# Performance work log

Measured on AMD Instinct MI355X. Metric: run time of the kernel, lower is better.

Reference implementation:

```python
import jax, jax.numpy as jnp
import numpy as np

DT = 0.01  # init kwarg dt
M = 501    # microstructure feature length (hardcoded split [501, 501] in source)
H = 128    # hidden width


def _mlp(x, W1, b1, W2, b2):
    # Linear -> Softplus -> Linear
    return jax.nn.softplus(x @ W1 + b1) @ W2 + b2


def _linear_init(key, fan_in, fan_out):
    k1, k2 = jax.random.split(key)
    s = 1.0 / np.sqrt(fan_in)
    W = jax.random.uniform(k1, (fan_in, fan_out), minval=-s, maxval=s, dtype=jnp.float32)
    b = jax.random.uniform(k2, (fan_out,), minval=-s, maxval=s, dtype=jnp.float32)
    return W, b


def setup_inputs() -> dict:
    key = jax.random.key(0)
    ks = jax.random.split(key, 10)
    B, T = 32768, 512
    Ew1, Eb1 = _linear_init(ks[0], 2 * M, H)   # energy net: Linear(1002,128)
    Ew2, Eb2 = _linear_init(ks[1], H, 1)
    nw1, nb1 = _linear_init(ks[2], M, H)       # nu net: Linear(501,128)
    nw2, nb2 = _linear_init(ks[3], H, 1)
    bw1, bb1 = _linear_init(ks[4], 2 * M, H)   # beta net: Linear(1002,128)
    bw2, bb2 = _linear_init(ks[5], H, 1)
    e = jax.random.normal(ks[6], (B, T, 1), dtype=jnp.float32) * 0.01
    e_dot = jax.random.normal(ks[7], (B, T, 1), dtype=jnp.float32) * 0.01
    E = jax.random.uniform(ks[8], (B, M), dtype=jnp.float32)
    nu = jax.random.uniform(ks[9], (B, M), dtype=jnp.float32)
    return dict(e=e, e_dot=e_dot, E=E, nu=nu,
                Ew1=Ew1, Eb1=Eb1, Ew2=Ew2, Eb2=Eb2,
                nw1=nw1, nb1=nb1, nw2=nw2, nb2=nb2,
                bw1=bw1, bb1=bb1, bw2=bw2, bb2=bb2)


def reference(e, e_dot, E, nu,
              Ew1, Eb1, Ew2, Eb2,
              nw1, nb1, nw2, nb2,
              bw1, bb1, bw2, bb2):
    # microstructure encoder: m = concat(E, nu) -> [B, 1002]; constant over time,
    # so the three small MLPs are evaluated ONCE (the per-step autograd.grad of the
    # quadratic energy/dissipation potentials has closed form).
    m = jnp.concatenate((E, nu), axis=-1)
    Emod = jnp.exp(_mlp(m, Ew1, Eb1, Ew2, Eb2))                              # exp(E(m))    [B,1]
    nu_feat = m[:, M:]                                                        # second half of split
    nuv = jnp.exp(jnp.square(_mlp(nu_feat, nw1, nb1, nw2, nb2)) / 40000.0)    # exp(nu(.))   [B,1]
    beta = jnp.square(_mlp(m, bw1, bb1, bw2, bb2)) / 40000.0                  # beta(m)      [B,1]

    # Per-step closed-form derivatives of
    #   energy    = 1/2 exp(E(m)) u^2 + 1/2 (u - v)^2        (u = e_t, v = xi_t)
    #   potential = -1/2 exp(nu) p^2 + 1/2 sum(beta q^2)     (p = e_dot_t, q = -dE/dv = e_t - xi_t)
    #   s_eq = exp(E) u + (u - v);  s_neq = dPhi/dp = -exp(nu) p;  kinetics = dPhi/dq = beta q
    def step(xi, inputs):
        et, edt = inputs                     # [B,1] each
        q = et - xi
        stress_t = Emod * et + q + nuv * edt  # s_eq - s_neq
        xi_next = xi + DT * beta * q
        return xi_next, (stress_t, xi)

    xi0 = jnp.zeros_like(e[:, 0])            # [B,1]
    eT = jnp.moveaxis(e, 1, 0)               # [T,B,1]
    edT = jnp.moveaxis(e_dot, 1, 0)
    _, (stress, xi) = jax.lax.scan(step, xi0, (eT, edT))
    return jnp.moveaxis(stress, 0, 1), jnp.moveaxis(xi, 0, 1)  # [B,T,1] each
```

## Files before the change

### kernel.cpp

```cpp
#include <hip/hip_runtime.h>
#include <hip/hip_bf16.h>

#define M_ 501
#define NTOT 384
#define T_ 512
#define DT_ 0.01f

typedef __attribute__((ext_vector_type(8))) __bf16 bf16x8;
typedef __attribute__((ext_vector_type(4))) float f32x4;

static __device__ __forceinline__ unsigned int pack2(float a, float b) {
    __hip_bfloat16 ha = __float2bfloat16(a);
    __hip_bfloat16 hb = __float2bfloat16(b);
    unsigned short ua = __builtin_bit_cast(unsigned short, ha);
    unsigned short ub = __builtin_bit_cast(unsigned short, hb);
    return (unsigned int)ua | ((unsigned int)ub << 16);
}

__global__ void build_w(const float* __restrict__ Ew1, const float* __restrict__ bw1,
                        const float* __restrict__ nw1, __hip_bfloat16* __restrict__ Wswz) {
    int idx = blockIdx.x * 256 + threadIdx.x;
    if (idx >= 32 * 24 * 64 * 8) return;
    int e  = idx & 7;
    int l  = (idx >> 3) & 63;
    int t  = idx >> 9;
    int nt = t % 24, k0 = t / 24;
    int k  = k0 * 32 + ((l >> 4) << 3) + e;
    int n  = nt * 16 + (l & 15);
    float v = 0.f;
    if (n < 128)      { if (k < 2*M_)             v = Ew1[k * 128 + n]; }
    else if (n < 256) { if (k < 2*M_)             v = bw1[k * 128 + (n - 128)]; }
    else              { if (k >= M_ && k < 2*M_)  v = nw1[(k - M_) * 128 + (n - 256)]; }
    Wswz[idx] = __float2bfloat16(v);
}

__global__ __launch_bounds__(512, 4) void mlp_gemm_fused2(
    const float* __restrict__ E, const float* __restrict__ nu,
    const __hip_bfloat16* __restrict__ Wswz,
    const float* __restrict__ Eb1, const float* __restrict__ bb1, const float* __restrict__ nb1,
    const float* __restrict__ Ew2, const float* __restrict__ bw2, const float* __restrict__ nw2,
    const float* __restrict__ Eb2, const float* __restrict__ bb2, const float* __restrict__ nb2,
    float* __restrict__ Emod, float* __restrict__ nuv, float* __restrict__ beta, int B)
{
    const int tid = threadIdx.x;
    const int wid = tid >> 6, l = tid & 63;
    const int c = l & 15, g = l >> 4;
    const int brow = blockIdx.x * 32;

    __shared__ __align__(16) unsigned char sAraw[32 * 1024 * 2];

    #pragma unroll
    for (int it = 0; it < 8; ++it) {
        const int idx = tid + it * 512;
        const int r = idx >> 7, cu = idx & 127;
        const size_t rb = (size_t)(brow + r) * M_;
        float f0, f1, f2, f3, f4, f5, f6, f7;
        const bool slow = (cu == 62) | (cu >= 124);
        if (!slow) {
            const float* src = (cu < 62) ? E : nu;
            const int off = (cu < 62) ? cu * 8 : cu * 8 - M_;
            const size_t s = rb + (size_t)off;
            const int o = (int)(s & 3);
            const f32x4* p = (const f32x4*)(src + (s & ~(size_t)3));
            f32x4 q0 = p[0], q1 = p[1], q2 = p[2];
            asm volatile("" : "+v"(q0), "+v"(q1), "+v"(q2));
            float g0=q0[0], g1=q0[1], g2=q0[2], g3=q0[3],
                  g4=q1[0], g5=q1[1], g6=q1[2], g7=q1[3],
                  g8=q2[0], g9=q2[1], g10=q2[2];
            const bool o2 = (o & 2) != 0, o1 = (o & 1) != 0;
            float u0 = o2?g2:g0, u1 = o2?g3:g1, u2 = o2?g4:g2, u3 = o2?g5:g3,
                  u4 = o2?g6:g4, u5 = o2?g7:g5, u6 = o2?g8:g6, u7 = o2?g9:g7,
                  u8 = o2?g10:g8;
            f0 = o1?u1:u0; f1 = o1?u2:u1; f2 = o1?u3:u2; f3 = o1?u4:u3;
            f4 = o1?u5:u4; f5 = o1?u6:u5; f6 = o1?u7:u6; f7 = o1?u8:u7;
        } else {
            const int kb = cu * 8;
            auto ldx = [&](int k) -> float {
                return (k < M_) ? E[rb + k] : ((k < 2 * M_) ? nu[rb + k - M_] : 0.f);
            };
            f0 = ldx(kb+0); f1 = ldx(kb+1); f2 = ldx(kb+2); f3 = ldx(kb+3);
            f4 = ldx(kb+4); f5 = ldx(kb+5); f6 = ldx(kb+6); f7 = ldx(kb+7);
        }
        uint4 vv;
        vv.x = pack2(f0, f1); vv.y = pack2(f2, f3);
        vv.z = pack2(f4, f5); vv.w = pack2(f6, f7);
        const unsigned bo = ((unsigned)r << 11) + (((unsigned)cu << 4) ^ (((unsigned)(r & 7)) << 4));
        *(uint4*)(sAraw + bo) = vv;
    }
    __syncthreads();

    const bf16x8* wbase = (const bf16x8*)Wswz;
    f32x4 acc[2][3];
    #pragma unroll
    for (int mi = 0; mi < 2; mi++)
        #pragma unroll
        for (int nt = 0; nt < 3; nt++) acc[mi][nt] = (f32x4){0.f, 0.f, 0.f, 0.f};

    for (int k0 = 0; k0 < 32; ++k0) {
        bf16x8 af[2];
        #pragma unroll
        for (int mi = 0; mi < 2; mi++) {
            const int row = c + mi * 16;
            const unsigned bo = ((unsigned)row << 11) +
                ((((unsigned)k0 << 6) + ((unsigned)g << 4)) ^ (((unsigned)(row & 7)) << 4));
            af[mi] = *(const bf16x8*)(sAraw + bo);
        }
        #pragma unroll
        for (int nt = 0; nt < 3; nt++) {
            bf16x8 bfrag = wbase[(size_t)(k0 * 24 + wid * 3 + nt) * 64 + l];
            #pragma unroll
            for (int mi = 0; mi < 2; mi++)
                acc[mi][nt] = __builtin_amdgcn_mfma_f32_16x16x32_bf16(af[mi], bfrag, acc[mi][nt], 0, 0, 0);
        }
    }
    __syncthreads();

    float* lds_s = (float*)sAraw;
    if (tid < 96) lds_s[tid] = 0.f;
    __syncthreads();

    #pragma unroll
    for (int nt = 0; nt < 3; nt++) {
        int gnt = wid * 3 + nt;
        int mlp = gnt >> 3;
        int jj = (gnt * 16 + c) & 127;
        float b1 = (mlp == 0) ? Eb1[jj] : (mlp == 1) ? bb1[jj] : nb1[jj];
        float w2 = (mlp == 0) ? Ew2[jj] : (mlp == 1) ? bw2[jj] : nw2[jj];
        #pragma unroll
        for (int mi = 0; mi < 2; mi++) {
            #pragma unroll
            for (int r = 0; r < 4; r++) {
                float x = acc[mi][nt][r] + b1;
                float h = fmaxf(x, 0.f) + __logf(1.f + __expf(-fabsf(x)));
                float v = h * w2;
                v += __shfl_xor(v, 1);
                v += __shfl_xor(v, 2);
                v += __shfl_xor(v, 4);
                v += __shfl_xor(v, 8);
                if (c == 0) atomicAdd(&lds_s[mlp * 32 + mi * 16 + g * 4 + r], v);
            }
        }
    }
    __syncthreads();

    if (tid < 32) {
        int b = brow + tid;
        float s0 = lds_s[tid], s1 = lds_s[32 + tid], s2 = lds_s[64 + tid];
        Emod[b] = __expf(s0 + Eb2[0]);
        float mb = s1 + bb2[0];
        beta[b]  = mb * mb * (1.f / 40000.f);
        float mn = s2 + nb2[0];
        nuv[b]   = __expf(mn * mn * (1.f / 40000.f));
    }
}

__global__ __launch_bounds__(256) void scan_k(
    const float* __restrict__ e, const float* __restrict__ ed,
    const float* __restrict__ Emod, const float* __restrict__ nuv, const float* __restrict__ beta,
    float* __restrict__ stress, float* __restrict__ xiout)
{
    int lane = threadIdx.x & 63;
    int b = blockIdx.x * 4 + (threadIdx.x >> 6);
    float Em = Emod[b], nv = nuv[b], bt = beta[b];
    float cc = DT_ * bt;
    float a  = 1.f - cc;

    size_t base = (size_t)b * T_ + (size_t)lane * 8;
    float4 e0 = *(const float4*)(e + base),  e1 = *(const float4*)(e + base + 4);
    float4 d0 = *(const float4*)(ed + base), d1 = *(const float4*)(ed + base + 4);
    float ev[8] = {e0.x, e0.y, e0.z, e0.w, e1.x, e1.y, e1.z, e1.w};
    float dv[8] = {d0.x, d0.y, d0.z, d0.w, d1.x, d1.y, d1.z, d1.w};

    float S = 0.f;
    #pragma unroll
    for (int j = 0; j < 8; j++) S = a * S + ev[j];
    float a2 = a * a, a4 = a2 * a2, A = a4 * a4;

    #pragma unroll
    for (int d = 1; d < 64; d <<= 1) {
        float Su = __shfl_up(S, d);
        float Au = __shfl_up(A, d);
        if (lane >= d) { S = Su * A + S; A = Au * A; }
    }
    float Sp = __shfl_up(S, 1);
    float xi = (lane == 0) ? 0.f : cc * Sp;

    float st[8], xo[8];
    #pragma unroll
    for (int j = 0; j < 8; j++) {
        xo[j] = xi;
        float q = ev[j] - xi;
        st[j] = Em * ev[j] + q + nv * dv[j];
        xi = xi + cc * q;
    }
    *(float4*)(stress + base)     = (float4){st[0], st[1], st[2], st[3]};
    *(float4*)(stress + base + 4) = (float4){st[4], st[5], st[6], st[7]};
    *(float4*)(xiout + base)      = (float4){xo[0], xo[1], xo[2], xo[3]};
    *(float4*)(xiout + base + 4)  = (float4){xo[4], xo[5], xo[6], xo[7]};
}

extern "C" void kernel_launch(void* const* d_in, const int* in_sizes, int n_in,
                              void* d_out, int out_size, void* d_ws, size_t ws_size,
                              hipStream_t stream) {
    const float* e   = (const float*)d_in[0];
    const float* ed  = (const float*)d_in[1];
    const float* E   = (const float*)d_in[2];
    const float* nu  = (const float*)d_in[3];
    const float* Ew1 = (const float*)d_in[4];
    const float* Eb1 = (const float*)d_in[5];
    const float* Ew2 = (const float*)d_in[6];
    const float* Eb2 = (const float*)d_in[7];
    const float* nw1 = (const float*)d_in[8];
    const float* nb1 = (const float*)d_in[9];
    const float* nw2 = (const float*)d_in[10];
    const float* nb2 = (const float*)d_in[11];
    const float* bw1 = (const float*)d_in[12];
    const float* bb1 = (const float*)d_in[13];
    const float* bw2 = (const float*)d_in[14];
    const float* bb2 = (const float*)d_in[15];

    int B = in_sizes[2] / M_;

    char* ws = (char*)d_ws;
    __hip_bfloat16* Wswz = (__hip_bfloat16*)ws;
    float* Emod = (float*)(ws + (size_t)1024 * NTOT * 2);
    float* nuv  = Emod + B;
    float* beta = nuv + B;

    build_w<<<(1024 * NTOT + 255) / 256, 256, 0, stream>>>(Ew1, bw1, nw1, Wswz);
    mlp_gemm_fused2<<<B / 32, 512, 0, stream>>>(E, nu, Wswz, Eb1, bb1, nb1,
                                                Ew2, bw2, nw2, Eb2, bb2, nb2,
                                                Emod, nuv, beta, B);
    float* stress = (float*)d_out;
    float* xiout  = stress + (size_t)B * T_;
    scan_k<<<B / 4, 256, 0, stream>>>(e, ed, Emod, nuv, beta, stress, xiout);
}
```

Baseline: 130.5 us.

## Enlarge GEMM row tile to 128 with double-buffered K-chunk staging

The MLP GEMM kernel now processes 128 rows per block instead of 32, so each weight fragment loaded from global memory is reused across 8 row tiles rather than 2. The A operand is staged through LDS in double-buffered 128-column chunks, with the next chunk's global loads issued while the current chunk's MFMAs run. The epilogue keeps the bias and second-layer weights in LDS and reduces across lanes with fewer shuffles. The cost is more accumulator registers (occupancy hint lowered to 2) and a quarter as many blocks.

```diff
diff --git a/kernel.cpp b/kernel.cpp
--- a/kernel.cpp
+++ b/kernel.cpp
@@ -2,7 +2,6 @@
 #include <hip/hip_bf16.h>
 
 #define M_ 501
-#define NTOT 384
 #define T_ 512
 #define DT_ 0.01f
 
@@ -34,7 +33,7 @@
     Wswz[idx] = __float2bfloat16(v);
 }
 
-__global__ __launch_bounds__(512, 4) void mlp_gemm_fused2(
+__global__ __launch_bounds__(512, 2) void mlp_gemm3(
     const float* __restrict__ E, const float* __restrict__ nu,
     const __hip_bfloat16* __restrict__ Wswz,
     const float* __restrict__ Eb1, const float* __restrict__ bb1, const float* __restrict__ nb1,
@@ -45,107 +44,161 @@
     const int tid = threadIdx.x;
     const int wid = tid >> 6, l = tid & 63;
     const int c = l & 15, g = l >> 4;
-    const int brow = blockIdx.x * 32;
-
-    __shared__ __align__(16) unsigned char sAraw[32 * 1024 * 2];
-
-    #pragma unroll
-    for (int it = 0; it < 8; ++it) {
-        const int idx = tid + it * 512;
-        const int r = idx >> 7, cu = idx & 127;
-        const size_t rb = (size_t)(brow + r) * M_;
-        float f0, f1, f2, f3, f4, f5, f6, f7;
-        const bool slow = (cu == 62) | (cu >= 124);
-        if (!slow) {
-            const float* src = (cu < 62) ? E : nu;
-            const int off = (cu < 62) ? cu * 8 : cu * 8 - M_;
-            const size_t s = rb + (size_t)off;
-            const int o = (int)(s & 3);
-            const f32x4* p = (const f32x4*)(src + (s & ~(size_t)3));
-            f32x4 q0 = p[0], q1 = p[1], q2 = p[2];
-            asm volatile("" : "+v"(q0), "+v"(q1), "+v"(q2));
-            float g0=q0[0], g1=q0[1], g2=q0[2], g3=q0[3],
-                  g4=q1[0], g5=q1[1], g6=q1[2], g7=q1[3],
-                  g8=q2[0], g9=q2[1], g10=q2[2];
-            const bool o2 = (o & 2) != 0, o1 = (o & 1) != 0;
+    const int brow = blockIdx.x * 128;
+
+    __shared__ __align__(16) unsigned char sAraw[2][128 * 256];
+    __shared__ float cb1[384], cw2[384];
+    __shared__ float lds_s[3][128];
+
+    if (tid < 384) {
+        int n = tid;
+        cb1[n] = (n < 128) ? Eb1[n] : (n < 256) ? bb1[n - 128] : nb1[n - 256];
+        cw2[n] = (n < 128) ? Ew2[n] : (n < 256) ? bw2[n - 128] : nw2[n - 256];
+        ((float*)lds_s)[n] = 0.f;
+    }
+
+    f32x4 q[12]; int ofs[4];
+    auto stage_load = [&](int ch) {
+        #pragma unroll
+        for (int j = 0; j < 4; ++j) {
+            int idx = tid + j * 512;
+            int r = idx >> 4, u = idx & 15;
+            int cu = ch * 16 + u;
+            size_t rb = (size_t)(brow + r) * M_;
+            bool slow = (cu == 62) | (cu >= 124);
+            if (!slow) {
+                const float* src = (cu < 62) ? E : nu;
+                int off = (cu < 62) ? cu * 8 : cu * 8 - M_;
+                size_t s = rb + (size_t)off;
+                ofs[j] = (int)(s & 3);
+                const f32x4* p = (const f32x4*)(src + (s & ~(size_t)3));
+                q[3*j] = p[0]; q[3*j+1] = p[1]; q[3*j+2] = p[2];
+                asm volatile("" : "+v"(q[3*j]), "+v"(q[3*j+1]), "+v"(q[3*j+2]));
+            } else {
+                int kb = cu * 8;
+                auto ldx = [&](int k) -> float {
+                    return (k < M_) ? E[rb + k] : ((k < 2 * M_) ? nu[rb + k - M_] : 0.f);
+                };
+                q[3*j]   = (f32x4){ldx(kb+0), ldx(kb+1), ldx(kb+2), ldx(kb+3)};
+                q[3*j+1] = (f32x4){ldx(kb+4), ldx(kb+5), ldx(kb+6), ldx(kb+7)};
+                q[3*j+2] = (f32x4){0.f, 0.f, 0.f, 0.f};
+                ofs[j] = 0;
+            }
+        }
+    };
+    auto stage_finish = [&](int nbuf) {
+        #pragma unroll
+        for (int j = 0; j < 4; ++j) {
+            int idx = tid + j * 512;
+            int r = idx >> 4, u = idx & 15;
+            float g0 = q[3*j][0],   g1 = q[3*j][1],   g2 = q[3*j][2],   g3 = q[3*j][3],
+                  g4 = q[3*j+1][0], g5 = q[3*j+1][1], g6 = q[3*j+1][2], g7 = q[3*j+1][3],
+                  g8 = q[3*j+2][0], g9 = q[3*j+2][1], g10 = q[3*j+2][2];
+            const bool o2 = (ofs[j] & 2) != 0, o1 = (ofs[j] & 1) != 0;
             float u0 = o2?g2:g0, u1 = o2?g3:g1, u2 = o2?g4:g2, u3 = o2?g5:g3,
                   u4 = o2?g6:g4, u5 = o2?g7:g5, u6 = o2?g8:g6, u7 = o2?g9:g7,
                   u8 = o2?g10:g8;
-            f0 = o1?u1:u0; f1 = o1?u2:u1; f2 = o1?u3:u2; f3 = o1?u4:u3;
-            f4 = o1?u5:u4; f5 = o1?u6:u5; f6 = o1?u7:u6; f7 = o1?u8:u7;
-        } else {
-            const int kb = cu * 8;
-            auto ldx = [&](int k) -> float {
-                return (k < M_) ? E[rb + k] : ((k < 2 * M_) ? nu[rb + k - M_] : 0.f);
-            };
-            f0 = ldx(kb+0); f1 = ldx(kb+1); f2 = ldx(kb+2); f3 = ldx(kb+3);
-            f4 = ldx(kb+4); f5 = ldx(kb+5); f6 = ldx(kb+6); f7 = ldx(kb+7);
-        }
-        uint4 vv;
-        vv.x = pack2(f0, f1); vv.y = pack2(f2, f3);
-        vv.z = pack2(f4, f5); vv.w = pack2(f6, f7);
-        const unsigned bo = ((unsigned)r << 11) + (((unsigned)cu << 4) ^ (((unsigned)(r & 7)) << 4));
-        *(uint4*)(sAraw + bo) = vv;
-    }
+            float f0 = o1?u1:u0, f1 = o1?u2:u1, f2 = o1?u3:u2, f3 = o1?u4:u3,
+                  f4 = o1?u5:u4, f5 = o1?u6:u5, f6 = o1?u7:u6, f7 = o1?u8:u7;
+            uint4 vv;
+            vv.x = pack2(f0, f1); vv.y = pack2(f2, f3);
+            vv.z = pack2(f4, f5); vv.w = pack2(f6, f7);
+            unsigned bo = ((unsigned)r << 8) + ((((unsigned)u) << 4) ^ (((unsigned)(r & 7)) << 4));
+            *(uint4*)(sAraw[nbuf] + bo) = vv;
+        }
+    };
+
+    const bf16x8* wbase = (const bf16x8*)Wswz;
+    auto loadW3 = [&](bf16x8 (&w)[3], int kg) {
+        #pragma unroll
+        for (int nt = 0; nt < 3; ++nt)
+            w[nt] = wbase[(size_t)(kg * 24 + wid * 3 + nt) * 64 + l];
+    };
+
+    f32x4 acc[8][3];
+    #pragma unroll
+    for (int mi = 0; mi < 8; mi++)
+        #pragma unroll
+        for (int nt = 0; nt < 3; nt++) acc[mi][nt] = (f32x4){0.f, 0.f, 0.f, 0.f};
+    bf16x8 wa[3], wb[3], af[8];
+
+    auto readAF = [&](int buf, int k0) {
+        #pragma unroll
+        for (int mi = 0; mi < 8; ++mi) {
+            int row = c + mi * 16;
+            unsigned bo = ((unsigned)row << 8) +
+                ((((unsigned)k0 << 6) + ((unsigned)g << 4)) ^ (((unsigned)(row & 7)) << 4));
+            af[mi] = *(const bf16x8*)(sAraw[buf] + bo);
+        }
+    };
+    auto M24 = [&](bf16x8 (&w)[3]) {
+        #pragma unroll
+        for (int nt = 0; nt < 3; ++nt)
+            #pragma unroll
+            for (int mi = 0; mi < 8; ++mi)
+                acc[mi][nt] = __builtin_amdgcn_mfma_f32_16x16x32_bf16(w[nt], af[mi], acc[mi][nt], 0, 0, 0);
+    };
+
+    stage_load(0);
+    stage_finish(0);
     __syncthreads();
 
-    const bf16x8* wbase = (const bf16x8*)Wswz;
-    f32x4 acc[2][3];
-    #pragma unroll
-    for (int mi = 0; mi < 2; mi++)
-        #pragma unroll
-        for (int nt = 0; nt < 3; nt++) acc[mi][nt] = (f32x4){0.f, 0.f, 0.f, 0.f};
-
-    for (int k0 = 0; k0 < 32; ++k0) {
-        bf16x8 af[2];
-        #pragma unroll
-        for (int mi = 0; mi < 2; mi++) {
-            const int row = c + mi * 16;
-            const unsigned bo = ((unsigned)row << 11) +
-                ((((unsigned)k0 << 6) + ((unsigned)g << 4)) ^ (((unsigned)(row & 7)) << 4));
-            af[mi] = *(const bf16x8*)(sAraw + bo);
-        }
-        #pragma unroll
-        for (int nt = 0; nt < 3; nt++) {
-            bf16x8 bfrag = wbase[(size_t)(k0 * 24 + wid * 3 + nt) * 64 + l];
+    for (int ch = 0; ch < 8; ++ch) {
+        const int buf = ch & 1;
+        if (ch < 7) stage_load(ch + 1);
+        const int kg = ch * 4;
+        loadW3(wa, kg + 0);
+        loadW3(wb, kg + 1);
+        readAF(buf, 0); M24(wa);
+        loadW3(wa, kg + 2);
+        readAF(buf, 1); M24(wb);
+        loadW3(wb, kg + 3);
+        readAF(buf, 2); M24(wa);
+        readAF(buf, 3); M24(wb);
+        if (ch < 7) stage_finish(buf ^ 1);
+        __syncthreads();
+    }
+
+    float bv[12], wv[12];
+    #pragma unroll
+    for (int nt = 0; nt < 3; ++nt)
+        #pragma unroll
+        for (int r = 0; r < 4; ++r) {
+            int nidx = (wid * 3 + nt) * 16 + g * 4 + r;
+            bv[nt * 4 + r] = cb1[nidx];
+            wv[nt * 4 + r] = cw2[nidx];
+        }
+    const int m_first = (wid * 3) >> 3, m_last = (wid * 3 + 2) >> 3;
+
+    #pragma unroll
+    for (int mi = 0; mi < 8; ++mi) {
+        float s0 = 0.f, s1 = 0.f, s2 = 0.f;
+        #pragma unroll
+        for (int nt = 0; nt < 3; ++nt) {
+            float p = 0.f;
             #pragma unroll
-            for (int mi = 0; mi < 2; mi++)
-                acc[mi][nt] = __builtin_amdgcn_mfma_f32_16x16x32_bf16(af[mi], bfrag, acc[mi][nt], 0, 0, 0);
-        }
+            for (int r = 0; r < 4; ++r) {
+                float x = acc[mi][nt][r] + bv[nt * 4 + r];
+                float h = fmaxf(x, 0.f) + __logf(1.f + __expf(-fabsf(x)));
+                p += h * wv[nt * 4 + r];
+            }
+            int m = (wid * 3 + nt) >> 3;
+            if (m == 0) s0 += p; else if (m == 1) s1 += p; else s2 += p;
+        }
+        auto red = [&](float v, int m) {
+            v += __shfl_xor(v, 16);
+            v += __shfl_xor(v, 32);
+            if (l < 16) atomicAdd(&lds_s[m][mi * 16 + l], v);
+        };
+        if (m_first == 0) red(s0, 0);
+        if (m_first <= 1 && m_last >= 1) red(s1, 1);
+        if (m_last == 2) red(s2, 2);
     }
     __syncthreads();
 
-    float* lds_s = (float*)sAraw;
-    if (tid < 96) lds_s[tid] = 0.f;
-    __syncthreads();
-
-    #pragma unroll
-    for (int nt = 0; nt < 3; nt++) {
-        int gnt = wid * 3 + nt;
-        int mlp = gnt >> 3;
-        int jj = (gnt * 16 + c) & 127;
-        float b1 = (mlp == 0) ? Eb1[jj] : (mlp == 1) ? bb1[jj] : nb1[jj];
-        float w2 = (mlp == 0) ? Ew2[jj] : (mlp == 1) ? bw2[jj] : nw2[jj];
-        #pragma unroll
-        for (int mi = 0; mi < 2; mi++) {
-            #pragma unroll
-            for (int r = 0; r < 4; r++) {
-                float x = acc[mi][nt][r] + b1;
-                float h = fmaxf(x, 0.f) + __logf(1.f + __expf(-fabsf(x)));
-                float v = h * w2;
-                v += __shfl_xor(v, 1);
-                v += __shfl_xor(v, 2);
-                v += __shfl_xor(v, 4);
-                v += __shfl_xor(v, 8);
-                if (c == 0) atomicAdd(&lds_s[mlp * 32 + mi * 16 + g * 4 + r], v);
-            }
-        }
-    }
-    __syncthreads();
-
-    if (tid < 32) {
+    if (tid < 128) {
         int b = brow + tid;
-        float s0 = lds_s[tid], s1 = lds_s[32 + tid], s2 = lds_s[64 + tid];
+        float s0 = lds_s[0][tid], s1 = lds_s[1][tid], s2 = lds_s[2][tid];
         Emod[b] = __expf(s0 + Eb2[0]);
         float mb = s1 + bb2[0];
         beta[b]  = mb * mb * (1.f / 40000.f);
@@ -189,9 +242,9 @@
     #pragma unroll
     for (int j = 0; j < 8; j++) {
         xo[j] = xi;
-        float q = ev[j] - xi;
-        st[j] = Em * ev[j] + q + nv * dv[j];
-        xi = xi + cc * q;
+        float qd = ev[j] - xi;
+        st[j] = Em * ev[j] + qd + nv * dv[j];
+        xi = xi + cc * qd;
     }
     *(float4*)(stress + base)     = (float4){st[0], st[1], st[2], st[3]};
     *(float4*)(stress + base + 4) = (float4){st[4], st[5], st[6], st[7]};
@@ -223,14 +276,14 @@
 
     char* ws = (char*)d_ws;
     __hip_bfloat16* Wswz = (__hip_bfloat16*)ws;
-    float* Emod = (float*)(ws + (size_t)1024 * NTOT * 2);
+    float* Emod = (float*)(ws + (size_t)1024 * 384 * 2);
     float* nuv  = Emod + B;
     float* beta = nuv + B;
 
-    build_w<<<(1024 * NTOT + 255) / 256, 256, 0, stream>>>(Ew1, bw1, nw1, Wswz);
-    mlp_gemm_fused2<<<B / 32, 512, 0, stream>>>(E, nu, Wswz, Eb1, bb1, nb1,
-                                                Ew2, bw2, nw2, Eb2, bb2, nb2,
-                                                Emod, nuv, beta, B);
+    build_w<<<(1024 * 384 + 255) / 256, 256, 0, stream>>>(Ew1, bw1, nw1, Wswz);
+    mlp_gemm3<<<B / 128, 512, 0, stream>>>(E, nu, Wswz, Eb1, bb1, nb1,
+                                           Ew2, bw2, nw2, Eb2, bb2, nb2,
+                                           Emod, nuv, beta, B);
     float* stress = (float*)d_out;
     float* xiout  = stress + (size_t)B * T_;
     scan_k<<<B / 4, 256, 0, stream>>>(e, ed, Emod, nuv, beta, stress, xiout);
```

After: 115.5 us. -11.5%, faster.
